# Optimization experiments

Hardware: AMD Instinct MI355X
Metric: run time of the kernel (lower is better)

Reference implementation:

```python
import jax, jax.numpy as jnp
import numpy as np

IN_FEATURES = 1024
N_CLASSES = 50257
CUTOFFS = [0, 5000, 20000, 50257]  # cluster boundaries (lows/highs)


def setup_inputs() -> dict:
    key = jax.random.key(0)
    ks = jax.random.split(key, 6)
    tokens = jax.random.randint(ks[0], (8, 4096), 0, N_CLASSES, dtype=jnp.int32)
    scale = 0.02
    head_emb = jax.random.normal(ks[1], (5000, IN_FEATURES), jnp.float32) * scale
    # tail cluster 0: hsz = 1024 // 2 = 512, osz = 20000 - 5000 = 15000
    tail0_emb = jax.random.normal(ks[2], (15000, 512), jnp.float32) * scale
    tail0_w = jax.random.normal(ks[3], (IN_FEATURES, 512), jnp.float32) * scale  # torch Linear weight (out, in)
    # tail cluster 1: hsz = 1024 // 4 = 256, osz = 50257 - 20000 = 30257
    tail1_emb = jax.random.normal(ks[4], (30257, 256), jnp.float32) * scale
    tail1_w = jax.random.normal(ks[5], (IN_FEATURES, 256), jnp.float32) * scale
    return {"tokens": tokens, "head_emb": head_emb, "tail0_emb": tail0_emb,
            "tail0_w": tail0_w, "tail1_emb": tail1_emb, "tail1_w": tail1_w}


def reference(tokens, head_emb, tail0_emb, tail0_w, tail1_emb, tail1_w):
    # AdaptiveInput forward (eval mode: Dropout = identity).
    # Each token id falls in exactly one cluster [low, high); lookup in that
    # cluster's table (shifted by low), project tails to in_features, scatter
    # back. We express gather+scatter as masked adds (clusters are disjoint).
    B, S = tokens.shape
    t = tokens.reshape(-1)  # [N]

    def cluster_out(low, high, table, w=None):
        mask = ((t >= low) & (t < high))[:, None]                 # [N, 1]
        idx = jnp.clip(t - low, 0, table.shape[0] - 1)            # in-range gather
        e = table[idx]                                            # [N, hsz]
        if w is not None:
            e = e @ w.T                                           # [N, in_features]
        return jnp.where(mask, e, jnp.zeros((), e.dtype))

    out = cluster_out(CUTOFFS[0], CUTOFFS[1], head_emb)
    out = out + cluster_out(CUTOFFS[1], CUTOFFS[2], tail0_emb, tail0_w)
    out = out + cluster_out(CUTOFFS[2], CUTOFFS[3], tail1_emb, tail1_w)
    return out.reshape(B, S, IN_FEATURES)
```

## Files before the change

### kernel.cpp

```cpp
#include <hip/hip_runtime.h>
#include <hip/hip_bf16.h>


typedef __attribute__((ext_vector_type(8))) short short8;
typedef __attribute__((ext_vector_type(4))) float f32x4;
typedef unsigned int u32;
typedef unsigned short u16;

__device__ __forceinline__ u32 pk2bf(float a, float b) {
    __hip_bfloat162 h = __float22bfloat162_rn(make_float2(a, b));
    union { __hip_bfloat162 h; u32 u; } c; c.h = h; return c.u;
}

__device__ __forceinline__ void glds16(const void* g, void* l) {
    __builtin_amdgcn_global_load_lds((const __attribute__((address_space(1))) u32*)g,
                                     (__attribute__((address_space(3))) u32*)l, 16, 0, 0);
}

__global__ __launch_bounds__(256) void ai_prep(
    const float* __restrict__ s0, const float* __restrict__ s1,
    const float* __restrict__ s2, const float* __restrict__ s3,
    u16* __restrict__ d0, u16* __restrict__ d1,
    u16* __restrict__ d2, u16* __restrict__ d3,
    int c0, int c1, int c2, int c3,
    int* __restrict__ cnt, int do_cvt)
{
    if (blockIdx.x == 0 && threadIdx.x < 8) cnt[threadIdx.x] = 0;
    if (!do_cvt) return;
    int total = c0 + c1 + c2 + c3;
    for (int i = blockIdx.x * blockDim.x + threadIdx.x; i < total;
         i += gridDim.x * blockDim.x) {
        const float* s; u16* d; int j = i;
        if (j < c0)              { s = s0; d = d0; }
        else if ((j -= c0) < c1) { s = s1; d = d1; }
        else if ((j -= c1) < c2) { s = s2; d = d2; }
        else          { j -= c2;   s = s3; d = d3; }
        float4 a = *(const float4*)(s + (size_t)j * 8);
        float4 b = *(const float4*)(s + (size_t)j * 8 + 4);
        uint4 q = { pk2bf(a.x, a.y), pk2bf(a.z, a.w), pk2bf(b.x, b.y), pk2bf(b.z, b.w) };
        *(uint4*)(d + (size_t)j * 8) = q;
    }
}

__global__ __launch_bounds__(256) void ai_partition(const int* __restrict__ tokens, int n,
                                                    int* __restrict__ cnt,
                                                    int* __restrict__ l0, int* __restrict__ l1) {
    __shared__ int wcnt[4][3];
    __shared__ int wbase[4][3];
    int i = blockIdx.x * blockDim.x + threadIdx.x;
    int lane = threadIdx.x & 63, w = threadIdx.x >> 6;
    int t = (i < n) ? tokens[i] : -1;
    int c = (t < 0) ? 3 : (t >= 20000) ? 1 : (t >= 5000) ? 0 : 2;
    unsigned long long m0 = __ballot(c == 0);
    unsigned long long m1 = __ballot(c == 1);
    unsigned long long m2 = __ballot(c == 2);
    if (lane == 0) { wcnt[w][0] = __popcll(m0); wcnt[w][1] = __popcll(m1); wcnt[w][2] = __popcll(m2); }
    __syncthreads();
    if (threadIdx.x < 3) {
        int j = threadIdx.x;
        int s0 = wcnt[0][j], s1 = wcnt[1][j], s2 = wcnt[2][j], s3 = wcnt[3][j];
        int base = atomicAdd(&cnt[j], s0 + s1 + s2 + s3);
        wbase[0][j] = base; wbase[1][j] = base + s0;
        wbase[2][j] = base + s0 + s1; wbase[3][j] = base + s0 + s1 + s2;
    }
    __syncthreads();
    unsigned long long lt = (1ull << lane) - 1ull;
    if (c == 0)      l0[wbase[w][0] + __popcll(m0 & lt)] = i;
    else if (c == 1) l1[wbase[w][1] + __popcll(m1 & lt)] = i;
    else if (c == 2) l1[n - 1 - (wbase[w][2] + __popcll(m2 & lt))] = i;
}

__global__ __launch_bounds__(256) void ai_head_copy(const int* __restrict__ tokens,
                                                    const int* __restrict__ l1, int n,
                                                    const int* __restrict__ cnt,
                                                    const float* __restrict__ emb,
                                                    float* __restrict__ out) {
    const int hc = cnt[2];
    for (int m = blockIdx.x; m < hc; m += gridDim.x) {
        int p = l1[n - 1 - m];
        int t = tokens[p];
        const float4* src = (const float4*)(emb + (size_t)t * 1024);
        float4* dst = (float4*)(out + (size_t)p * 1024);
        dst[threadIdx.x] = src[threadIdx.x];
    }
}

template<bool PRE>
__global__ __launch_bounds__(256) void ai_tail_gemm(
    const int* __restrict__ tokens,
    const int* __restrict__ l0, const int* __restrict__ l1,
    const int* __restrict__ cnt,
    const float* __restrict__ e0f, const float* __restrict__ e1f,
    const float* __restrict__ w0f, const float* __restrict__ w1f,
    const u16* __restrict__ e0b, const u16* __restrict__ e1b,
    const u16* __restrict__ w0b, const u16* __restrict__ w1b,
    float* __restrict__ out)
{
    constexpr int BK = 64;
    __shared__ __align__(16) u16 As[2][128 * BK];
    __shared__ __align__(16) u16 Bs[2][128 * BK];
    __shared__ int s_erow[128];
    __shared__ int s_opos[128];

    const int z = blockIdx.z;
    const int K     = z ? 256 : 512;
    const int low   = z ? 20000 : 5000;
    const int count = cnt[z];
    const int* list = z ? l1 : l0;
    const float* ef = z ? e1f : e0f;
    const float* wf = z ? w1f : w0f;
    const u16*   eb = z ? e1b : e0b;
    const u16*   wb = z ? w1b : w0b;

    const int id = blockIdx.y * 8 + blockIdx.x;
    const int xcd = id & 7, q = id >> 3;
    const int m0 = (((q >> 3) << 3) | xcd) * 128;
    const int n0 = (q & 7) * 128;
    if (m0 >= count) return;
    const int tid = threadIdx.x;

    if (tid < 128) {
        int m = m0 + tid;
        if (m < count) {
            int p = list[m];
            s_opos[tid] = p;
            s_erow[tid] = tokens[p] - low;
        } else {
            s_opos[tid] = -1;
            s_erow[tid] = -1;
        }
    }
    __syncthreads();

    f32x4 acc[4][4];
    #pragma unroll
    for (int i = 0; i < 4; i++)
        #pragma unroll
        for (int j = 0; j < 4; j++)
            acc[i][j] = (f32x4){0.f, 0.f, 0.f, 0.f};

    const int lane = tid & 63;
    const int wave = tid >> 6;
    const int wm = (wave >> 1) * 64;
    const int wn = (wave & 1) * 64;
    const int fr = lane & 15;
    const int fk = (lane >> 4) * 8;
    const int swzm = (fr & 7) << 4;

    const int rlc  = lane >> 3;
    const int c16s = (lane & 7) ^ rlc;

    const u16* aSrc[4];
    const u16* bSrc[4];
    if (PRE) {
        #pragma unroll
        for (int i = 0; i < 4; i++) {
            int row = (wave * 4 + i) * 8 + rlc;
            int er = s_erow[row]; if (er < 0) er = 0;
            aSrc[i] = eb + (size_t)er * K + c16s * 8;
            bSrc[i] = wb + (size_t)(n0 + row) * K + c16s * 8;
        }
    }

    const int srow  = tid >> 1;
    const int shalf = tid & 1;
    const int er32 = s_erow[srow];
    float4 areg[8], breg[8];

    auto issue = [&](int kt, int buf) {
        if (PRE) {
            #pragma unroll
            for (int i = 0; i < 4; i++) {
                int chunk = wave * 4 + i;
                glds16(aSrc[i] + kt, &As[buf][chunk * 512]);
                glds16(bSrc[i] + kt, &Bs[buf][chunk * 512]);
            }
        } else {
            if (er32 >= 0) {
                const float4* src = (const float4*)(ef + (size_t)er32 * K + kt + shalf * 32);
                #pragma unroll
                for (int j = 0; j < 8; j++) areg[j] = src[j];
            }
            const float4* srcB = (const float4*)(wf + (size_t)(n0 + srow) * K + kt + shalf * 32);
            #pragma unroll
            for (int j = 0; j < 8; j++) breg[j] = srcB[j];
        }
    };
    auto publish = [&](int buf) {
        if (!PRE) {
            int sm = (srow & 7) << 4;
            char* baseA = (char*)&As[buf][0] + srow * 128;
            char* baseB = (char*)&Bs[buf][0] + srow * 128;
            #pragma unroll
            for (int j = 0; j < 4; j++) {
                uint4 qa;
                if (er32 >= 0)
                    qa = (uint4){ pk2bf(areg[2*j].x, areg[2*j].y), pk2bf(areg[2*j].z, areg[2*j].w),
                                  pk2bf(areg[2*j+1].x, areg[2*j+1].y), pk2bf(areg[2*j+1].z, areg[2*j+1].w) };
                else qa = (uint4){0u, 0u, 0u, 0u};
                uint4 qb = { pk2bf(breg[2*j].x, breg[2*j].y), pk2bf(breg[2*j].z, breg[2*j].w),
                             pk2bf(breg[2*j+1].x, breg[2*j+1].y), pk2bf(breg[2*j+1].z, breg[2*j+1].w) };
                *(uint4*)(baseA + ((shalf * 64 + j * 16) ^ sm)) = qa;
                *(uint4*)(baseB + ((shalf * 64 + j * 16) ^ sm)) = qb;
            }
        }
    };

    auto compute = [&](int buf) {
        const char* Abase = (const char*)&As[buf][0];
        const char* Bbase = (const char*)&Bs[buf][0];
        #pragma unroll
        for (int kk = 0; kk < BK; kk += 32) {
            short8 af[4], bf[4];
            #pragma unroll
            for (int f = 0; f < 4; f++) {
                int ra = wm + f * 16 + fr;
                int rb = wn + f * 16 + fr;
                int cb = ((kk + fk) << 1);
                af[f] = *(const short8*)(Abase + ra * 128 + (cb ^ ((ra & 7) << 4)));
                bf[f] = *(const short8*)(Bbase + rb * 128 + (cb ^ ((rb & 7) << 4)));
            }
            #pragma unroll
            for (int i = 0; i < 4; i++)
                #pragma unroll
                for (int j = 0; j < 4; j++)
                    acc[i][j] = __builtin_amdgcn_mfma_f32_16x16x32_bf16(af[i], bf[j], acc[i][j], 0, 0, 0);
        }
    };

    issue(0, 0);
    publish(0);
    __syncthreads();

    const int nt = K / BK;
    for (int t = 0; t < nt; t++) {
        const int cur = t & 1;
        const bool more = (t + 1 < nt);
        if (more) issue((t + 1) * BK, cur ^ 1);
        compute(cur);
        __syncthreads();
        if (more) {
            publish(cur ^ 1);
            if (!PRE) __syncthreads();
        }
    }

    const int rbase = (lane >> 4) * 4;
    #pragma unroll
    for (int i = 0; i < 4; i++) {
        #pragma unroll
        for (int r = 0; r < 4; r++) {
            int ml = wm + i * 16 + rbase + r;
            if (m0 + ml < count) {
                float* orow = out + (size_t)s_opos[ml] * 1024 + n0 + wn + fr;
                orow[0]  = acc[i][0][r];
                orow[16] = acc[i][1][r];
                orow[32] = acc[i][2][r];
                orow[48] = acc[i][3][r];
            }
        }
    }
}

extern "C" void kernel_launch(void* const* d_in, const int* in_sizes, int n_in,
                              void* d_out, int out_size, void* d_ws, size_t ws_size,
                              hipStream_t stream) {
    const int*   tokens   = (const int*)d_in[0];
    const float* head_emb = (const float*)d_in[1];
    const float* t0_emb   = (const float*)d_in[2];
    const float* t0_w     = (const float*)d_in[3];
    const float* t1_emb   = (const float*)d_in[4];
    const float* t1_w     = (const float*)d_in[5];
    float* out = (float*)d_out;
    const int N = in_sizes[0];
    const int nE0 = in_sizes[2];
    const int nW0 = in_sizes[3];
    const int nE1 = in_sizes[4];
    const int nW1 = in_sizes[5];

    int* cnt = (int*)d_ws;
    int* l0  = cnt + 16;
    int* l1  = l0 + N;
    size_t base_need = 64 + (size_t)2 * N * 4;
    size_t tbl_elems = (size_t)nW0 + nW1 + nE0 + nE1;
    bool pre = ws_size >= base_need + tbl_elems * 2;
    u16* wb0 = (u16*)((char*)d_ws + base_need);
    u16* wb1 = wb0 + nW0;
    u16* eb0 = wb1 + nW1;
    u16* eb1 = eb0 + nE0;

    ai_prep<<<2048, 256, 0, stream>>>(t0_w, t1_w, t0_emb, t1_emb,
                                      wb0, wb1, eb0, eb1,
                                      nW0 / 8, nW1 / 8, nE0 / 8, nE1 / 8,
                                      cnt, pre ? 1 : 0);
    ai_partition<<<(N + 255) / 256, 256, 0, stream>>>(tokens, N, cnt, l0, l1);
    ai_head_copy<<<1024, 256, 0, stream>>>(tokens, l1, N, cnt, head_emb, out);

    dim3 g(8, (N + 127) / 128, 2);
    if (pre)
        ai_tail_gemm<true><<<g, 256, 0, stream>>>(tokens, l0, l1, cnt,
                                                  t0_emb, t1_emb, t0_w, t1_w,
                                                  eb0, eb1, wb0, wb1, out);
    else
        ai_tail_gemm<false><<<g, 256, 0, stream>>>(tokens, l0, l1, cnt,
                                                   t0_emb, t1_emb, t0_w, t1_w,
                                                   eb0, eb1, wb0, wb1, out);
}
```

Baseline: 250.7 us.

## Gather and convert only used embedding rows to packed bf16 before GEMM

```diff
diff --git a/kernel.cpp b/kernel.cpp
--- a/kernel.cpp
+++ b/kernel.cpp
@@ -15,31 +15,6 @@
 __device__ __forceinline__ void glds16(const void* g, void* l) {
     __builtin_amdgcn_global_load_lds((const __attribute__((address_space(1))) u32*)g,
                                      (__attribute__((address_space(3))) u32*)l, 16, 0, 0);
-}
-
-__global__ __launch_bounds__(256) void ai_prep(
-    const float* __restrict__ s0, const float* __restrict__ s1,
-    const float* __restrict__ s2, const float* __restrict__ s3,
-    u16* __restrict__ d0, u16* __restrict__ d1,
-    u16* __restrict__ d2, u16* __restrict__ d3,
-    int c0, int c1, int c2, int c3,
-    int* __restrict__ cnt, int do_cvt)
-{
-    if (blockIdx.x == 0 && threadIdx.x < 8) cnt[threadIdx.x] = 0;
-    if (!do_cvt) return;
-    int total = c0 + c1 + c2 + c3;
-    for (int i = blockIdx.x * blockDim.x + threadIdx.x; i < total;
-         i += gridDim.x * blockDim.x) {
-        const float* s; u16* d; int j = i;
-        if (j < c0)              { s = s0; d = d0; }
-        else if ((j -= c0) < c1) { s = s1; d = d1; }
-        else if ((j -= c1) < c2) { s = s2; d = d2; }
-        else          { j -= c2;   s = s3; d = d3; }
-        float4 a = *(const float4*)(s + (size_t)j * 8);
-        float4 b = *(const float4*)(s + (size_t)j * 8 + 4);
-        uint4 q = { pk2bf(a.x, a.y), pk2bf(a.z, a.w), pk2bf(b.x, b.y), pk2bf(b.z, b.w) };
-        *(uint4*)(d + (size_t)j * 8) = q;
-    }
 }
 
 __global__ __launch_bounds__(256) void ai_partition(const int* __restrict__ tokens, int n,
@@ -70,6 +45,53 @@
     else if (c == 2) l1[n - 1 - (wbase[w][2] + __popcll(m2 & lt))] = i;
 }
 
+__global__ __launch_bounds__(256) void ai_gather_cvt(
+    const int* __restrict__ tokens,
+    const int* __restrict__ l0, const int* __restrict__ l1,
+    const int* __restrict__ cnt, int n,
+    const float* __restrict__ e0f, const float* __restrict__ e1f,
+    const float* __restrict__ w0f, const float* __restrict__ w1f,
+    u16* __restrict__ a0p, u16* __restrict__ a1p,
+    u16* __restrict__ wb0, u16* __restrict__ wb1)
+{
+    const int c0 = cnt[0], c1 = cnt[1];
+    const int wItems = (1024 * 512 + 1024 * 256) / 8;
+    const int i1 = wItems + n * 64;
+    const int total = i1 + n * 32;
+    for (int i = blockIdx.x * blockDim.x + threadIdx.x; i < total;
+         i += gridDim.x * blockDim.x) {
+        const float* s; u16* d; size_t so, dofs;
+        if (i < wItems) {
+            int j = i;
+            if (j < 65536) { s = w0f; d = wb0; so = (size_t)j * 8; }
+            else           { s = w1f; d = wb1; so = (size_t)(j - 65536) * 8; }
+            dofs = so;
+        } else if (i < i1) {
+            int j = i - wItems;
+            int m = j >> 6;
+            if (m >= c0) continue;
+            int k8 = j & 63;
+            int er = tokens[l0[m]] - 5000;
+            s = e0f; d = a0p;
+            so = (size_t)er * 512 + k8 * 8;
+            dofs = (size_t)m * 512 + k8 * 8;
+        } else {
+            int j = i - i1;
+            int m = j >> 5;
+            if (m >= c1) continue;
+            int k8 = j & 31;
+            int er = tokens[l1[m]] - 20000;
+            s = e1f; d = a1p;
+            so = (size_t)er * 256 + k8 * 8;
+            dofs = (size_t)m * 256 + k8 * 8;
+        }
+        float4 a = *(const float4*)(s + so);
+        float4 b = *(const float4*)(s + so + 4);
+        uint4 q = { pk2bf(a.x, a.y), pk2bf(a.z, a.w), pk2bf(b.x, b.y), pk2bf(b.z, b.w) };
+        *(uint4*)(d + dofs) = q;
+    }
+}
+
 __global__ __launch_bounds__(256) void ai_head_copy(const int* __restrict__ tokens,
                                                     const int* __restrict__ l1, int n,
                                                     const int* __restrict__ cnt,
@@ -85,32 +107,24 @@
     }
 }
 
-template<bool PRE>
 __global__ __launch_bounds__(256) void ai_tail_gemm(
-    const int* __restrict__ tokens,
     const int* __restrict__ l0, const int* __restrict__ l1,
     const int* __restrict__ cnt,
-    const float* __restrict__ e0f, const float* __restrict__ e1f,
-    const float* __restrict__ w0f, const float* __restrict__ w1f,
-    const u16* __restrict__ e0b, const u16* __restrict__ e1b,
-    const u16* __restrict__ w0b, const u16* __restrict__ w1b,
+    const u16* __restrict__ a0p, const u16* __restrict__ a1p,
+    const u16* __restrict__ wb0, const u16* __restrict__ wb1,
     float* __restrict__ out)
 {
     constexpr int BK = 64;
     __shared__ __align__(16) u16 As[2][128 * BK];
     __shared__ __align__(16) u16 Bs[2][128 * BK];
-    __shared__ int s_erow[128];
     __shared__ int s_opos[128];
 
     const int z = blockIdx.z;
     const int K     = z ? 256 : 512;
-    const int low   = z ? 20000 : 5000;
     const int count = cnt[z];
     const int* list = z ? l1 : l0;
-    const float* ef = z ? e1f : e0f;
-    const float* wf = z ? w1f : w0f;
-    const u16*   eb = z ? e1b : e0b;
-    const u16*   wb = z ? w1b : w0b;
+    const u16* ap   = z ? a1p : a0p;
+    const u16* wb   = z ? wb1 : wb0;
 
     const int id = blockIdx.y * 8 + blockIdx.x;
     const int xcd = id & 7, q = id >> 3;
@@ -118,26 +132,6 @@
     const int n0 = (q & 7) * 128;
     if (m0 >= count) return;
     const int tid = threadIdx.x;
-
-    if (tid < 128) {
-        int m = m0 + tid;
-        if (m < count) {
-            int p = list[m];
-            s_opos[tid] = p;
-            s_erow[tid] = tokens[p] - low;
-        } else {
-            s_opos[tid] = -1;
-            s_erow[tid] = -1;
-        }
-    }
-    __syncthreads();
-
-    f32x4 acc[4][4];
-    #pragma unroll
-    for (int i = 0; i < 4; i++)
-        #pragma unroll
-        for (int j = 0; j < 4; j++)
-            acc[i][j] = (f32x4){0.f, 0.f, 0.f, 0.f};
 
     const int lane = tid & 63;
     const int wave = tid >> 6;
@@ -152,59 +146,36 @@
 
     const u16* aSrc[4];
     const u16* bSrc[4];
-    if (PRE) {
+    #pragma unroll
+    for (int i = 0; i < 4; i++) {
+        int row = (wave * 4 + i) * 8 + rlc;
+        int ar = m0 + row; if (ar >= count) ar = count - 1;
+        aSrc[i] = ap + (size_t)ar * K + c16s * 8;
+        bSrc[i] = wb + (size_t)(n0 + row) * K + c16s * 8;
+    }
+
+    auto issue = [&](int kt, int buf) {
         #pragma unroll
         for (int i = 0; i < 4; i++) {
-            int row = (wave * 4 + i) * 8 + rlc;
-            int er = s_erow[row]; if (er < 0) er = 0;
-            aSrc[i] = eb + (size_t)er * K + c16s * 8;
-            bSrc[i] = wb + (size_t)(n0 + row) * K + c16s * 8;
-        }
-    }
-
-    const int srow  = tid >> 1;
-    const int shalf = tid & 1;
-    const int er32 = s_erow[srow];
-    float4 areg[8], breg[8];
-
-    auto issue = [&](int kt, int buf) {
-        if (PRE) {
-            #pragma unroll
-            for (int i = 0; i < 4; i++) {
-                int chunk = wave * 4 + i;
-                glds16(aSrc[i] + kt, &As[buf][chunk * 512]);
-                glds16(bSrc[i] + kt, &Bs[buf][chunk * 512]);
-            }
-        } else {
-            if (er32 >= 0) {
-                const float4* src = (const float4*)(ef + (size_t)er32 * K + kt + shalf * 32);
-                #pragma unroll
-                for (int j = 0; j < 8; j++) areg[j] = src[j];
-            }
-            const float4* srcB = (const float4*)(wf + (size_t)(n0 + srow) * K + kt + shalf * 32);
-            #pragma unroll
-            for (int j = 0; j < 8; j++) breg[j] = srcB[j];
+            int chunk = wave * 4 + i;
+            glds16(aSrc[i] + kt, &As[buf][chunk * 512]);
+            glds16(bSrc[i] + kt, &Bs[buf][chunk * 512]);
         }
     };
-    auto publish = [&](int buf) {
-        if (!PRE) {
-            int sm = (srow & 7) << 4;
-            char* baseA = (char*)&As[buf][0] + srow * 128;
-            char* baseB = (char*)&Bs[buf][0] + srow * 128;
-            #pragma unroll
-            for (int j = 0; j < 4; j++) {
-                uint4 qa;
-                if (er32 >= 0)
-                    qa = (uint4){ pk2bf(areg[2*j].x, areg[2*j].y), pk2bf(areg[2*j].z, areg[2*j].w),
-                                  pk2bf(areg[2*j+1].x, areg[2*j+1].y), pk2bf(areg[2*j+1].z, areg[2*j+1].w) };
-                else qa = (uint4){0u, 0u, 0u, 0u};
-                uint4 qb = { pk2bf(breg[2*j].x, breg[2*j].y), pk2bf(breg[2*j].z, breg[2*j].w),
-                             pk2bf(breg[2*j+1].x, breg[2*j+1].y), pk2bf(breg[2*j+1].z, breg[2*j+1].w) };
-                *(uint4*)(baseA + ((shalf * 64 + j * 16) ^ sm)) = qa;
-                *(uint4*)(baseB + ((shalf * 64 + j * 16) ^ sm)) = qb;
-            }
-        }
-    };
+
+    f32x4 acc[4][4];
+    #pragma unroll
+    for (int i = 0; i < 4; i++)
+        #pragma unroll
+        for (int j = 0; j < 4; j++)
+            acc[i][j] = (f32x4){0.f, 0.f, 0.f, 0.f};
+
+    issue(0, 0);
+
+    if (tid < 128) {
+        int m = m0 + tid;
+        s_opos[tid] = (m < count) ? list[m] : -1;
+    }
 
     auto compute = [&](int buf) {
         const char* Abase = (const char*)&As[buf][0];
@@ -216,9 +187,9 @@
             for (int f = 0; f < 4; f++) {
                 int ra = wm + f * 16 + fr;
                 int rb = wn + f * 16 + fr;
-                int cb = ((kk + fk) << 1);
-                af[f] = *(const short8*)(Abase + ra * 128 + (cb ^ ((ra & 7) << 4)));
-                bf[f] = *(const short8*)(Bbase + rb * 128 + (cb ^ ((rb & 7) << 4)));
+                int cb = ((kk + fk) << 1) ^ swzm;
+                af[f] = *(const short8*)(Abase + ra * 128 + cb);
+                bf[f] = *(const short8*)(Bbase + rb * 128 + cb);
             }
             #pragma unroll
             for (int i = 0; i < 4; i++)
@@ -228,21 +199,19 @@
         }
     };
 
-    issue(0, 0);
-    publish(0);
-    __syncthreads();
-
     const int nt = K / BK;
     for (int t = 0; t < nt; t++) {
         const int cur = t & 1;
-        const bool more = (t + 1 < nt);
-        if (more) issue((t + 1) * BK, cur ^ 1);
+        if (t + 1 < nt) {
+            issue((t + 1) * BK, cur ^ 1);
+            asm volatile("s_waitcnt vmcnt(8)" ::: "memory");
+        } else {
+            asm volatile("s_waitcnt vmcnt(0)" ::: "memory");
+        }
+        __builtin_amdgcn_s_barrier();
         compute(cur);
-        __syncthreads();
-        if (more) {
-            publish(cur ^ 1);
-            if (!PRE) __syncthreads();
-        }
+        asm volatile("" ::: "memory");
+        __builtin_amdgcn_s_barrier();
     }
 
     const int rbase = (lane >> 4) * 4;
@@ -262,6 +231,37 @@
     }
 }
 
+__global__ __launch_bounds__(256) void ai_naive(
+    const int* __restrict__ tokens,
+    const float* __restrict__ he,
+    const float* __restrict__ e0, const float* __restrict__ w0,
+    const float* __restrict__ e1, const float* __restrict__ w1,
+    float* __restrict__ out)
+{
+    int p = blockIdx.x;
+    int t = tokens[p];
+    float* o = out + (size_t)p * 1024;
+    if (t < 5000) {
+        for (int j = threadIdx.x; j < 1024; j += 256) o[j] = he[(size_t)t * 1024 + j];
+    } else if (t < 20000) {
+        const float* e = e0 + (size_t)(t - 5000) * 512;
+        for (int j = threadIdx.x; j < 1024; j += 256) {
+            float s = 0.f;
+            const float* wr = w0 + (size_t)j * 512;
+            for (int k = 0; k < 512; k++) s += e[k] * wr[k];
+            o[j] = s;
+        }
+    } else {
+        const float* e = e1 + (size_t)(t - 20000) * 256;
+        for (int j = threadIdx.x; j < 1024; j += 256) {
+            float s = 0.f;
+            const float* wr = w1 + (size_t)j * 256;
+            for (int k = 0; k < 256; k++) s += e[k] * wr[k];
+            o[j] = s;
+        }
+    }
+}
+
 extern "C" void kernel_launch(void* const* d_in, const int* in_sizes, int n_in,
                               void* d_out, int out_size, void* d_ws, size_t ws_size,
                               hipStream_t stream) {
@@ -273,36 +273,30 @@
     const float* t1_w     = (const float*)d_in[5];
     float* out = (float*)d_out;
     const int N = in_sizes[0];
-    const int nE0 = in_sizes[2];
     const int nW0 = in_sizes[3];
-    const int nE1 = in_sizes[4];
     const int nW1 = in_sizes[5];
 
     int* cnt = (int*)d_ws;
     int* l0  = cnt + 16;
     int* l1  = l0 + N;
     size_t base_need = 64 + (size_t)2 * N * 4;
-    size_t tbl_elems = (size_t)nW0 + nW1 + nE0 + nE1;
-    bool pre = ws_size >= base_need + tbl_elems * 2;
+    size_t need = base_need + ((size_t)nW0 + nW1 + (size_t)N * 512 + (size_t)N * 256) * 2;
+    if (ws_size < need) {
+        ai_naive<<<N, 256, 0, stream>>>(tokens, head_emb, t0_emb, t0_w, t1_emb, t1_w, out);
+        return;
+    }
     u16* wb0 = (u16*)((char*)d_ws + base_need);
     u16* wb1 = wb0 + nW0;
-    u16* eb0 = wb1 + nW1;
-    u16* eb1 = eb0 + nE0;
-
-    ai_prep<<<2048, 256, 0, stream>>>(t0_w, t1_w, t0_emb, t1_emb,
-                                      wb0, wb1, eb0, eb1,
-                                      nW0 / 8, nW1 / 8, nE0 / 8, nE1 / 8,
-                                      cnt, pre ? 1 : 0);
+    u16* a0p = wb1 + nW1;
+    u16* a1p = a0p + (size_t)N * 512;
+
+    hipMemsetAsync(cnt, 0, 64, stream);
     ai_partition<<<(N + 255) / 256, 256, 0, stream>>>(tokens, N, cnt, l0, l1);
+    ai_gather_cvt<<<2048, 256, 0, stream>>>(tokens, l0, l1, cnt, N,
+                                            t0_emb, t1_emb, t0_w, t1_w,
+                                            a0p, a1p, wb0, wb1);
     ai_head_copy<<<1024, 256, 0, stream>>>(tokens, l1, N, cnt, head_emb, out);
 
     dim3 g(8, (N + 127) / 128, 2);
-    if (pre)
-        ai_tail_gemm<true><<<g, 256, 0, stream>>>(tokens, l0, l1, cnt,
-                                                  t0_emb, t1_emb, t0_w, t1_w,
-                                                  eb0, eb1, wb0, wb1, out);
-    else
-        ai_tail_gemm<false><<<g, 256, 0, stream>>>(tokens, l0, l1, cnt,
-                                                   t0_emb, t1_emb, t0_w, t1_w,
-                                                   eb0, eb1, wb0, wb1, out);
-}
+    ai_tail_gemm<<<g, 256, 0, stream>>>(l0, l1, cnt, a0p, a1p, wb0, wb1, out);
+}
```

Measured after the change: 242.2 us. 1.04x faster.
